# Optimization experiments

Hardware: AMD Instinct MI355X
Metric: run time of the kernel (lower is better)

## Reference

```python
import math
import jax, jax.numpy as jnp
import numpy as np

WS = (8, 7, 7)   # window_size (d, h, w)
SS = (4, 3, 3)   # shift_size
NH = 4           # num_heads
DIM = 128


def _rel_position_index(ws):
    # [N*N] int index into the (2wd-1)(2wh-1)(2ww-1) bias table
    cd, ch, cw = np.arange(ws[0]), np.arange(ws[1]), np.arange(ws[2])
    coords = np.stack(np.meshgrid(cd, ch, cw, indexing='ij')).reshape(3, -1)  # [3, N]
    rel = (coords[:, :, None] - coords[:, None, :]).transpose(1, 2, 0)        # [N, N, 3]
    rel[..., 0] += ws[0] - 1
    rel[..., 1] += ws[1] - 1
    rel[..., 2] += ws[2] - 1
    rel[..., 0] *= (2 * ws[1] - 1) * (2 * ws[2] - 1)
    rel[..., 1] *= (2 * ws[2] - 1)
    return rel.sum(-1).reshape(-1)


def _rel_coords_table(ws):
    # [(2wd-1)(2wh-1)(2ww-1), 3] log-spaced continuous coords (Swin v2)
    rd = np.arange(-(ws[0] - 1), ws[0], dtype=np.float32)
    rh = np.arange(-(ws[1] - 1), ws[1], dtype=np.float32)
    rw = np.arange(-(ws[2] - 1), ws[2], dtype=np.float32)
    t = np.stack(np.meshgrid(rd, rh, rw, indexing='ij')).transpose(1, 2, 3, 0)  # [Td,Th,Tw,3]
    t[..., 0] /= ws[0] - 1
    t[..., 1] /= ws[1] - 1
    t[..., 2] /= ws[2] - 1
    t *= 8.0
    t = np.sign(t) * np.log2(np.abs(t) + 1.0) / 3.0
    return t.reshape(-1, 3)


_REL_INDEX = _rel_position_index(WS)
_COORDS = jnp.asarray(_rel_coords_table(WS))


def _attn_mask(pD, pH, pW, ws, ss):
    img = np.zeros((pD, pH, pW), np.float32)
    sl = lambda w, s: (slice(0, -w), slice(-w, -s), slice(-s, None))
    cnt = 0
    for d in sl(ws[0], ss[0]):
        for h in sl(ws[1], ss[1]):
            for w in sl(ws[2], ss[2]):
                img[d, h, w] = cnt
                cnt += 1
    m = img.reshape(pD // ws[0], ws[0], pH // ws[1], ws[1], pW // ws[2], ws[2])
    m = m.transpose(0, 2, 4, 1, 3, 5).reshape(-1, ws[0] * ws[1] * ws[2])  # [nWin, N]
    diff = m[:, None, :] - m[:, :, None]
    return jnp.asarray(np.where(diff != 0, -100.0, 0.0).astype(np.float32))


def setup_inputs() -> dict:
    key = jax.random.key(0)
    ks = jax.random.split(key, 6)
    B, D, H, W, C = 1, 16, 56, 56, DIM
    g = lambda k, shp, sc: jax.random.normal(k, shp, dtype=jnp.float32) * sc
    return {
        'x': g(ks[0], (B, D, H, W, C), 1.0),
        'qkv_weight': g(ks[1], (3 * C, C), 0.02),
        'qkv_bias': jnp.zeros((3 * C,), jnp.float32),
        'proj_weight': g(ks[2], (C, C), 0.02),
        'proj_bias': jnp.zeros((C,), jnp.float32),
        'logit_scale': jnp.full((NH, 1, 1), float(np.log(10.0)), jnp.float32),
        'cpb_w1': g(ks[3], (512, 3), 0.02),
        'cpb_b1': jnp.zeros((512,), jnp.float32),
        'cpb_w2': g(ks[4], (NH, 512), 0.02),
    }


def reference(x, qkv_weight, qkv_bias, proj_weight, proj_bias,
              logit_scale, cpb_w1, cpb_b1, cpb_w2):
    B, D, H, W, C = x.shape
    wd, wh, ww = WS
    hd = C // NH
    pad_d, pad_h, pad_w = (-D) % wd, (-H) % wh, (-W) % ww
    x = jnp.pad(x, ((0, 0), (0, pad_d), (0, pad_h), (0, pad_w), (0, 0)))
    pD, pH, pW = D + pad_d, H + pad_h, W + pad_w
    ss = [0 if WS[i] >= (pD, pH, pW)[i] else SS[i] for i in range(3)]
    shifted = sum(ss) > 0
    if shifted:
        x = jnp.roll(x, (-ss[0], -ss[1], -ss[2]), axis=(1, 2, 3))
    nd, nh, nw = pD // wd, pH // wh, pW // ww
    nWin, N = nd * nh * nw, wd * wh * ww
    # window partition -> [B*nWin, N, C]
    xw = x.reshape(B, nd, wd, nh, wh, nw, ww, C).transpose(0, 1, 3, 5, 2, 4, 6, 7)
    xw = xw.reshape(B * nWin, N, C)
    # qkv with k-bias zeroed (Swin v2 cosine attention)
    qb = qkv_bias.at[C:2 * C].set(0.0)
    qkv = (xw @ qkv_weight.T + qb).reshape(B * nWin, N, 3, NH, hd).transpose(2, 0, 3, 1, 4)
    q, k, v = qkv[0], qkv[1], qkv[2]   # each [B*nWin, NH, N, hd]
    qn = q / jnp.maximum(jnp.linalg.norm(q, axis=-1, keepdims=True), 1e-12)
    kn = k / jnp.maximum(jnp.linalg.norm(k, axis=-1, keepdims=True), 1e-12)
    attn = jnp.einsum('bhnd,bhmd->bhnm', qn, kn)
    scale = jnp.exp(jnp.minimum(logit_scale, math.log(100.0)))  # [NH,1,1]
    attn = attn * scale
    # continuous relative position bias
    table = jax.nn.relu(_COORDS @ cpb_w1.T + cpb_b1) @ cpb_w2.T  # [T, NH]
    bias = table[_REL_INDEX].reshape(N, N, NH).transpose(2, 0, 1)
    bias = 16.0 * jax.nn.sigmoid(bias)
    attn = attn + bias[None]
    if shifted:
        mask = _attn_mask(pD, pH, pW, WS, ss)  # [nWin, N, N]
        attn = attn.reshape(B, nWin, NH, N, N) + mask[None, :, None]
        attn = attn.reshape(B * nWin, NH, N, N)
    attn = jax.nn.softmax(attn, axis=-1)
    out = jnp.einsum('bhnm,bhmd->bhnd', attn, v).transpose(0, 2, 1, 3).reshape(B * nWin, N, C)
    out = out @ proj_weight.T + proj_bias
    # window reverse -> [B, pD, pH, pW, C]
    out = out.reshape(B, nd, nh, nw, wd, wh, ww, C).transpose(0, 1, 4, 2, 5, 3, 6, 7)
    out = out.reshape(B, pD, pH, pW, C)
    if shifted:
        out = jnp.roll(out, tuple(ss), axis=(1, 2, 3))
    return out[:, :D, :H, :W, :]
```

## Files before the change

kernel.cpp:

```cpp
#include <hip/hip_runtime.h>
#include <hip/hip_bf16.h>

typedef unsigned short u16;
typedef unsigned int   u32;
typedef float f32x4  __attribute__((ext_vector_type(4)));
typedef short bf16x8 __attribute__((ext_vector_type(8)));

#define DI __device__ __forceinline__

constexpr int TBL  = 2535;
constexpr int NTOK = 50176;
constexpr float L2E = 1.4426950408889634f;

constexpr int WB_QW = 0;
constexpr int WB_PW = 49152;
constexpr int WB_QB = 65536;
constexpr int WB_PB = 65920;
constexpr int WB_TOT = 66048;

DI float b2f(u16 u){ return __uint_as_float(((u32)u)<<16); }
DI u16 f2b(float f){
  u32 u = __float_as_uint(f);
  return (u16)((u + 0x7fffu + ((u>>16)&1u)) >> 16);
}
DI float ldf(const void* p, int i, int isf32){
  return isf32 ? ((const float*)p)[i] : b2f(((const u16*)p)[i]);
}
DI f32x4 mfma16(bf16x8 a, bf16x8 b, f32x4 c){
  return __builtin_amdgcn_mfma_f32_16x16x32_bf16(a, b, c, 0, 0, 0);
}
DI u32 cvtpk(float lo, float hi){
  u32 r;
  asm("v_cvt_pk_bf16_f32 %0, %1, %2" : "=v"(r) : "v"(lo), "v"(hi));
  return r;
}
DI float vexp2(float x){
  float r;
  asm("v_exp_f32 %0, %1" : "=v"(r) : "v"(x));
  return r;
}
DI int detect_f32(const void* x, int lane){
  u32 w = ((const u32*)x)[lane];
  u16 lo = (u16)w;
  u32 e = (lo >> 7) & 0xFF;
  int wild = (lo != 0 && (e >= 143 || e <= 111)) ? 1 : 0;
  unsigned long long m = __ballot(wild);
  return __popcll(m) > 16;
}

__global__ void k_cpb(const void* __restrict__ w1, const void* __restrict__ b1,
                      const void* __restrict__ w2, const void* __restrict__ x,
                      const void* __restrict__ qw, const void* __restrict__ pw,
                      const void* __restrict__ qb, const void* __restrict__ pb,
                      u16* __restrict__ wb, float* __restrict__ table16){
  const int lane = threadIdx.x;
  const int isf32 = detect_f32(x, lane);
  {
    int gid = blockIdx.x*64 + lane;
    if (gid < WB_TOT){
      const void* src; int off;
      if (gid < WB_PW)      { src = qw; off = gid; }
      else if (gid < WB_QB) { src = pw; off = gid - WB_PW; }
      else if (gid < WB_PB) { src = qb; off = gid - WB_QB; }
      else                  { src = pb; off = gid - WB_PB; }
      wb[gid] = isf32 ? f2b(((const float*)src)[off]) : ((const u16*)src)[off];
    }
  }
  int t = blockIdx.x;
  int i = t/169; int r = t - i*169; int j = r/13; int k = r - j*13;
  float v0 = 8.f*(float)(i-7)/7.f, v1 = 8.f*(float)(j-6)/6.f, v2 = 8.f*(float)(k-6)/6.f;
  float c0 = copysignf(log2f(fabsf(v0)+1.f)*(1.f/3.f), v0);
  float c1 = copysignf(log2f(fabsf(v1)+1.f)*(1.f/3.f), v1);
  float c2 = copysignf(log2f(fabsf(v2)+1.f)*(1.f/3.f), v2);
  float a0=0.f,a1=0.f,a2=0.f,a3=0.f;
  for (int hh = lane; hh < 512; hh += 64){
    float a = c0*ldf(w1,hh*3,isf32) + c1*ldf(w1,hh*3+1,isf32)
            + c2*ldf(w1,hh*3+2,isf32) + ldf(b1,hh,isf32);
    a = fmaxf(a, 0.f);
    a0 += a*ldf(w2,hh,isf32);       a1 += a*ldf(w2,512+hh,isf32);
    a2 += a*ldf(w2,1024+hh,isf32);  a3 += a*ldf(w2,1536+hh,isf32);
  }
  #pragma unroll
  for (int off=32; off; off>>=1){
    a0 += __shfl_xor(a0, off); a1 += __shfl_xor(a1, off);
    a2 += __shfl_xor(a2, off); a3 += __shfl_xor(a3, off);
  }
  if (lane==0){
    table16[t]       = (16.f/(1.f+__expf(-a0)) - 15.f)*L2E;
    table16[TBL+t]   = (16.f/(1.f+__expf(-a1)) - 15.f)*L2E;
    table16[2*TBL+t] = (16.f/(1.f+__expf(-a2)) - 15.f)*L2E;
    table16[3*TBL+t] = (16.f/(1.f+__expf(-a3)) - 15.f)*L2E;
  }
}

__global__ void k_bias(const float* __restrict__ table16, float* __restrict__ bias16){
  int n = blockIdx.x, h = blockIdx.y;
  int td = n/49; int r2 = n - td*49; int th = r2/7; int tw = r2 - th*7;
  const float* tb = table16 + h*TBL;
  float* o = bias16 + ((size_t)h*392 + n)*392;
  for (int m = threadIdx.x; m < 392; m += 128){
    int sd = m/49; int q2 = m - sd*49; int sh = q2/7; int sw = q2 - sh*7;
    int idx = (td - sd + 7)*169 + (th - sh + 6)*13 + (tw - sw + 6);
    o[m] = tb[idx];
  }
}

__global__ __launch_bounds__(256,3) void k_qkv(const void* __restrict__ x,
    const u16* __restrict__ wb, const void* __restrict__ lsc,
    u16* __restrict__ qkvbuf){
  __shared__ __align__(16) u16 As[64*136];
  __shared__ __align__(16) u16 Ws[128*136];
  const int tid = threadIdx.x;
  const int lane = tid & 63;
  const int isf32 = detect_f32(x, lane);
  const int tokbase0 = blockIdx.x*64;
  {
    int trow = tid>>2, cq = (tid&3)*32;
    int gtok = tokbase0 + trow;
    int win = gtok/392, tt = gtok - win*392;
    int dwi = win>>6, hwi = (win>>3)&7, wwi = win&7;
    int td = tt/49; int r2 = tt - td*49; int th = r2/7; int tw = r2 - th*7;
    int pd = dwi*8 + td + 4; if (pd >= 16) pd -= 16;
    int ph = hwi*7 + th + 3; if (ph >= 56) ph -= 56;
    int pw = wwi*7 + tw + 3; if (pw >= 56) pw -= 56;
    size_t pos = (size_t)((pd*56 + ph)*56 + pw)*128 + cq;
    if (isf32){
      const float4* src = (const float4*)((const float*)x + pos);
      #pragma unroll
      for (int u=0; u<8; ++u){
        float4 a = src[u];
        ushort4 s4 = make_ushort4(f2b(a.x), f2b(a.y), f2b(a.z), f2b(a.w));
        *(ushort4*)&As[trow*136 + cq + u*4] = s4;
      }
    } else {
      const uint4* src = (const uint4*)((const u16*)x + pos);
      #pragma unroll
      for (int u=0; u<4; ++u) *(uint4*)&As[trow*136 + cq + u*8] = src[u];
    }
  }
  const int wave = tid>>6;
  const int c = lane & 15, g = lane >> 4;
  float sl2e[4];
  #pragma unroll
  for (int h2=0; h2<4; ++h2){
    float ls = ldf(lsc, h2, isf32);
    sl2e[h2] = __expf(fminf(ls, 4.60517019f)) * L2E;
  }
  bf16x8 ka[4];
  for (int which = 0; which < 3; ++which){
    __syncthreads();
    {
      int orow = tid>>1, c2 = (tid&1)*64;
      const uint4* src = (const uint4*)(wb + WB_QW + (size_t)(which*128 + orow)*128 + c2);
      #pragma unroll
      for (int u=0; u<8; ++u) *(uint4*)&Ws[orow*136 + c2 + u*8] = src[u];
    }
    __syncthreads();
    if (which == 0){
      #pragma unroll
      for (int kk=0; kk<4; ++kk)
        ka[kk] = *(const bf16x8*)&As[(wave*16 + c)*136 + kk*32 + g*8];
    }
    f32x4 acc[8];
    #pragma unroll
    for (int nt=0; nt<8; ++nt) acc[nt] = 0.f;
    #pragma unroll
    for (int nt=0; nt<8; ++nt){
      #pragma unroll
      for (int kk=0; kk<4; ++kk){
        bf16x8 wf = *(const bf16x8*)&Ws[(nt*16 + c)*136 + kk*32 + g*8];
        acc[nt] = mfma16(ka[kk], wf, acc[nt]);
      }
    }
    if (which != 1){
      #pragma unroll
      for (int nt=0; nt<8; ++nt){
        float bv = b2f(wb[WB_QB + which*128 + nt*16 + c]);
        #pragma unroll
        for (int r=0;r<4;++r) acc[nt][r] += bv;
      }
    }
    if (which < 2){
      #pragma unroll
      for (int h2=0; h2<4; ++h2){
        f32x4 ss;
        #pragma unroll
        for (int r=0;r<4;++r)
          ss[r] = acc[2*h2][r]*acc[2*h2][r] + acc[2*h2+1][r]*acc[2*h2+1][r];
        #pragma unroll
        for (int off=1; off<16; off<<=1){
          #pragma unroll
          for (int r=0;r<4;++r) ss[r] += __shfl_xor(ss[r], off);
        }
        #pragma unroll
        for (int r=0;r<4;++r){
          float rn = rsqrtf(fmaxf(ss[r], 1e-24f));
          if (which == 0) rn *= sl2e[h2];
          acc[2*h2][r]   *= rn;
          acc[2*h2+1][r] *= rn;
        }
      }
    }
    __syncthreads();
    #pragma unroll
    for (int nt=0; nt<8; ++nt){
      #pragma unroll
      for (int r=0;r<4;++r)
        As[(wave*16 + 4*g + r)*136 + nt*16 + c] = f2b(acc[nt][r]);
    }
    __syncthreads();
    {
      const int tokl = tid>>2, seg = tid&3;
      u16* dst = qkvbuf + ((size_t)(which*4+seg)*NTOK + tokbase0 + tokl)*32;
      const u16* srcl = &As[tokl*136 + seg*32];
      #pragma unroll
      for (int u=0; u<4; ++u)
        *(uint4*)(dst + u*8) = *(const uint4*)(srcl + u*8);
    }
  }
}

DI bf16x8 ldK(const u16* klds, int jt, int c, int g){
  return *(const bf16x8*)&klds[(jt*16 + c)*40 + g*8];
}
DI float4 ldB(const float* brow, int jt, int g){
  int mbc = jt*16 + 4*g; if (mbc > 388) mbc = 388;
  return *(const float4*)(brow + mbc);
}
DI int4 ldC(const int* cnt, int jt, int g){
  int mbc = jt*16 + 4*g; if (mbc > 388) mbc = 388;
  return *(const int4*)&cnt[mbc];
}

#define QKT_BODY(JJ, TAIL, KF, BA, BB, CM, JT) do { \
  f32x4 tz = {0.f,0.f,0.f,0.f}; \
  f32x4 ta = mfma16(KF, qfa, tz); \
  f32x4 tb = mfma16(KF, qfb, tz); \
  float pa0 = vexp2(ta[0] + BA.x), pa1 = vexp2(ta[1] + BA.y); \
  float pa2 = vexp2(ta[2] + BA.z), pa3 = vexp2(ta[3] + BA.w); \
  float pb0 = vexp2(tb[0] + BB.x), pb1 = vexp2(tb[1] + BB.y); \
  float pb2 = vexp2(tb[2] + BB.z), pb3 = vexp2(tb[3] + BB.w); \
  if (MIXED){ \
    if (CM.x != cnA) pa0 = 0.f;  if (CM.y != cnA) pa1 = 0.f; \
    if (CM.z != cnA) pa2 = 0.f;  if (CM.w != cnA) pa3 = 0.f; \
    if (CM.x != cnB) pb0 = 0.f;  if (CM.y != cnB) pb1 = 0.f; \
    if (CM.z != cnB) pb2 = 0.f;  if (CM.w != cnB) pb3 = 0.f; \
  } \
  if (TAIL){ \
    const int mb = (JT)*16 + 4*g; \
    if (mb > 388){ pa0=0.f; pa1=0.f; pa2=0.f; pa3=0.f; \
                   pb0=0.f; pb1=0.f; pb2=0.f; pb3=0.f; } \
  } \
  uint2 wva, wvb; \
  wva.x = cvtpk(pa0,pa1); wva.y = cvtpk(pa2,pa3); \
  wvb.x = cvtpk(pb0,pb1); wvb.y = cvtpk(pb2,pb3); \
  *(uint2*)&psA[c*20 + (JJ)*8 + 2*g] = wva; \
  *(uint2*)&psB[c*20 + (JJ)*8 + 2*g] = wvb; \
} while(0)

#define PV_PAIR(MC) do { \
  bf16x8 pfa = *(const bf16x8*)&psA[c*20 + 4*g]; \
  bf16x8 pfb = *(const bf16x8*)&psB[c*20 + 4*g]; \
  bf16x8 va = *(const bf16x8*)&vT[c*424 + (MC)*32 + g*8]; \
  bf16x8 vb = *(const bf16x8*)&vT[(16+c)*424 + (MC)*32 + g*8]; \
  o0a = mfma16(va, pfa, o0a); o1a = mfma16(vb, pfa, o1a); o2a = mfma16(ones, pfa, o2a); \
  o0b = mfma16(va, pfb, o0b); o1b = mfma16(vb, pfb, o1b); o2b = mfma16(ones, pfb, o2b); \
} while(0)

template<bool MIXED>
DI void attn_main(const u16* __restrict__ qg, const float* __restrict__ bias_h,
                  const u16* klds, const u16* vT, u32* psA, u32* psB, const int* cnt,
                  u16* __restrict__ aout, int win, int h, int wave, int lane){
  const int c = lane & 15, g = lane >> 4;
  const short ob = 0x3F80;
  const bf16x8 ones = {ob,ob,ob,ob,ob,ob,ob,ob};
  const int4 zc = {0,0,0,0};
  for (int pp = wave; pp < 13; pp += 8){
    const int rta = 2*pp;
    const int rtb = (pp < 12) ? (2*pp+1) : 24;
    const bool hasB = (pp < 12);
    const int nbA = rta*16, nbB = rtb*16;
    const int ncA = (nbA + c < 392) ? (nbA + c) : 391;
    const int ncB = (nbB + c < 392) ? (nbB + c) : 391;
    const bf16x8 qfa = *(const bf16x8*)(qg + (size_t)ncA*32 + g*8);
    const bf16x8 qfb = *(const bf16x8*)(qg + (size_t)ncB*32 + g*8);
    const int cnA = MIXED ? cnt[ncA] : 0;
    const int cnB = MIXED ? cnt[ncB] : 0;
    const float* browA = bias_h + (size_t)ncA*392;
    const float* browB = bias_h + (size_t)ncB*392;
    f32x4 o0a = {0.f,0.f,0.f,0.f}, o1a = o0a, o2a = o0a;
    f32x4 o0b = o0a, o1b = o0a, o2b = o0a;
    bf16x8 kf0 = ldK(klds, 0, c, g);
    float4 ba0 = ldB(browA, 0, g), bb0 = ldB(browB, 0, g);
    int4   cm0 = MIXED ? ldC(cnt, 0, g) : zc;
    for (int mc = 0; mc < 12; ++mc){
      const int jt1 = 2*mc + 1, jt2 = 2*mc + 2;
      bf16x8 kf1 = ldK(klds, jt1, c, g);
      float4 ba1 = ldB(browA, jt1, g), bb1 = ldB(browB, jt1, g);
      int4   cm1 = MIXED ? ldC(cnt, jt1, g) : zc;
      QKT_BODY(0, false, kf0, ba0, bb0, cm0, 2*mc);
      kf0 = ldK(klds, jt2, c, g);
      ba0 = ldB(browA, jt2, g); bb0 = ldB(browB, jt2, g);
      cm0 = MIXED ? ldC(cnt, jt2, g) : zc;
      QKT_BODY(1, false, kf1, ba1, bb1, cm1, jt1);
      PV_PAIR(mc);
    }
    QKT_BODY(0, true, kf0, ba0, bb0, cm0, 24);
    { uint2 zz; zz.x = 0u; zz.y = 0u;
      *(uint2*)&psA[c*20 + 8 + 2*g] = zz;
      *(uint2*)&psB[c*20 + 8 + 2*g] = zz; }
    PV_PAIR(12);
    const float rva = 1.f / o2a[0];
    const float rvb = 1.f / o2b[0];
    uint2 wa, wb2;
    wa.x  = cvtpk(o0a[0]*rva, o0a[1]*rva);  wa.y  = cvtpk(o0a[2]*rva, o0a[3]*rva);
    wb2.x = cvtpk(o1a[0]*rva, o1a[1]*rva);  wb2.y = cvtpk(o1a[2]*rva, o1a[3]*rva);
    *(uint2*)&psA[c*20 + 2*g]     = wa;
    *(uint2*)&psA[c*20 + 8 + 2*g] = wb2;
    wa.x  = cvtpk(o0b[0]*rvb, o0b[1]*rvb);  wa.y  = cvtpk(o0b[2]*rvb, o0b[3]*rvb);
    wb2.x = cvtpk(o1b[0]*rvb, o1b[1]*rvb);  wb2.y = cvtpk(o1b[2]*rvb, o1b[3]*rvb);
    *(uint2*)&psB[c*20 + 2*g]     = wa;
    *(uint2*)&psB[c*20 + 8 + 2*g] = wb2;
    const int orow = lane>>2, oq = lane&3;
    uint4 ova = *(const uint4*)&psA[orow*20 + 4*oq];
    const int nA = nbA + orow;
    if (nA < 392)
      *(uint4*)(aout + ((size_t)(win*392 + nA))*128 + h*32 + oq*8) = ova;
    if (hasB){
      uint4 ovb = *(const uint4*)&psB[orow*20 + 4*oq];
      const int nB = nbB + orow;
      if (nB < 392)
        *(uint4*)(aout + ((size_t)(win*392 + nB))*128 + h*32 + oq*8) = ovb;
    }
  }
}

__global__ __launch_bounds__(512,4) void k_attn(const u16* __restrict__ qkv,
    const float* __restrict__ bias16, u16* __restrict__ aout){
  __shared__ __align__(16) u16 klds[400*40];
  __shared__ __align__(16) u16 vT[32*424];
  __shared__ __align__(16) u32 ps[8][640];
  __shared__ __align__(16) int cnt[400];
  const int tid = threadIdx.x;
  const int win = blockIdx.x, h = blockIdx.y;
  const int dwi = win>>6, hwi = (win>>3)&7, wwi = win&7;
  const u16* qg = qkv + ((size_t)(0*4 + h)*NTOK + (size_t)win*392)*32;
  const u16* kg = qkv + ((size_t)(1*4 + h)*NTOK + (size_t)win*392)*32;
  const u16* vg = qkv + ((size_t)(2*4 + h)*NTOK + (size_t)win*392)*32;
  for (int idx = tid; idx < 1600; idx += 512){
    const int row = idx>>2, q = idx&3;
    uint4 a = {0,0,0,0};
    if (row < 392) a = *(const uint4*)(kg + (size_t)row*32 + q*8);
    *(uint4*)&klds[row*40 + q*8] = a;
  }
  for (int idx = tid; idx < 784; idx += 512){
    const int mg = idx>>3, cg = idx&7;
    uint2 v0 = *(const uint2*)(vg + (size_t)(4*mg+0)*32 + cg*4);
    uint2 v1 = *(const uint2*)(vg + (size_t)(4*mg+1)*32 + cg*4);
    uint2 v2 = *(const uint2*)(vg + (size_t)(4*mg+2)*32 + cg*4);
    uint2 v3 = *(const uint2*)(vg + (size_t)(4*mg+3)*32 + cg*4);
    u16 e0[4], e1[4], e2[4], e3[4];
    e0[0]=(u16)v0.x; e0[1]=(u16)(v0.x>>16); e0[2]=(u16)v0.y; e0[3]=(u16)(v0.y>>16);
    e1[0]=(u16)v1.x; e1[1]=(u16)(v1.x>>16); e1[2]=(u16)v1.y; e1[3]=(u16)(v1.y>>16);
    e2[0]=(u16)v2.x; e2[1]=(u16)(v2.x>>16); e2[2]=(u16)v2.y; e2[3]=(u16)(v2.y>>16);
    e3[0]=(u16)v3.x; e3[1]=(u16)(v3.x>>16); e3[2]=(u16)v3.y; e3[3]=(u16)(v3.y>>16);
    #pragma unroll
    for (int cc=0; cc<4; ++cc){
      ushort4 w = make_ushort4(e0[cc], e1[cc], e2[cc], e3[cc]);
      *(ushort4*)&vT[(cg*4+cc)*424 + 4*mg] = w;
    }
  }
  for (int idx = tid; idx < 1024; idx += 512){
    int ch = idx>>5, mm = 392 + (idx&31);
    vT[ch*424 + mm] = 0;
  }
  for (int t2 = tid; t2 < 400; t2 += 512){
    int row = (t2 < 392) ? t2 : 391;
    int td = row/49; int r2 = row - td*49; int th = r2/7; int tw = r2 - th*7;
    int gd = dwi*8 + td, gh = hwi*7 + th, gw = wwi*7 + tw;
    int rd = (gd < 8) ? 0 : ((gd < 12) ? 1 : 2);
    int rh = (gh < 49) ? 0 : ((gh < 53) ? 1 : 2);
    int rw = (gw < 49) ? 0 : ((gw < 53) ? 1 : 2);
    cnt[t2] = rd*9 + rh*3 + rw;
  }
  __syncthreads();
  const int wave = tid>>6, lane = tid&63;
  u32* psA = &ps[wave][0];
  u32* psB = &ps[wave][320];
  const float* bias_h = bias16 + (size_t)h*153664;
  const bool uniform = (dwi == 0) && (hwi < 7) && (wwi < 7);
  if (uniform)
    attn_main<false>(qg, bias_h, klds, vT, psA, psB, cnt, aout, win, h, wave, lane);
  else
    attn_main<true >(qg, bias_h, klds, vT, psA, psB, cnt, aout, win, h, wave, lane);
}

__global__ __launch_bounds__(256,2) void k_proj(const u16* __restrict__ ain,
    const u16* __restrict__ wb, const void* __restrict__ x, void* __restrict__ out){
  __shared__ __align__(16) u16 As[64*136];
  __shared__ __align__(16) u16 Ws[128*136];
  const int tid = threadIdx.x;
  const int lane = tid & 63;
  const int isf32 = detect_f32(x, lane);
  const int tokbase0 = blockIdx.x*64;
  {
    int trow = tid>>2, cq = (tid&3)*32;
    const uint4* src = (const uint4*)(ain + (size_t)(tokbase0+trow)*128 + cq);
    #pragma unroll
    for (int u=0; u<4; ++u) *(uint4*)&As[trow*136 + cq + u*8] = src[u];
  }
  {
    int orow = tid>>1, c2 = (tid&1)*64;
    const uint4* src = (const uint4*)(wb + WB_PW + (size_t)orow*128 + c2);
    #pragma unroll
    for (int u=0; u<8; ++u) *(uint4*)&Ws[orow*136 + c2 + u*8] = src[u];
  }
  __syncthreads();
  const int wave = tid>>6;
  const int c = lane & 15, g = lane >> 4;
  bf16x8 ka[4];
  #pragma unroll
  for (int kk=0; kk<4; ++kk)
    ka[kk] = *(const bf16x8*)&As[(wave*16 + c)*136 + kk*32 + g*8];
  f32x4 acc[8];
  #pragma unroll
  for (int nt=0; nt<8; ++nt) acc[nt] = 0.f;
  #pragma unroll
  for (int nt=0; nt<8; ++nt){
    #pragma unroll
    for (int kk=0; kk<4; ++kk){
      bf16x8 wf = *(const bf16x8*)&Ws[(nt*16 + c)*136 + kk*32 + g*8];
      acc[nt] = mfma16(ka[kk], wf, acc[nt]);
    }
  }
  if (isf32){
    __syncthreads();
    float* WsF = (float*)Ws;
    #pragma unroll
    for (int nt=0; nt<8; ++nt){
      float bv = b2f(wb[WB_PB + nt*16 + c]);
      #pragma unroll
      for (int r=0;r<4;++r)
        WsF[(wave*16 + 4*g + r)*128 + nt*16 + c] = acc[nt][r] + bv;
    }
    __syncthreads();
    const int tok = tid>>2, q4 = tid&3;
    int gtok = tokbase0 + tok;
    int win = gtok/392, tt = gtok - win*392;
    int dwi = win>>6, hwi = (win>>3)&7, wwi = win&7;
    int td = tt/49; int r2 = tt - td*49; int th = r2/7; int tw = r2 - th*7;
    int pd = dwi*8 + td + 4; if (pd >= 16) pd -= 16;
    int ph = hwi*7 + th + 3; if (ph >= 56) ph -= 56;
    int pwx = wwi*7 + tw + 3; if (pwx >= 56) pwx -= 56;
    size_t po = (size_t)((pd*56 + ph)*56 + pwx)*128;
    const float4* srcv = (const float4*)&WsF[tok*128 + q4*32];
    float4* dst = (float4*)((float*)out + po + q4*32);
    #pragma unroll
    for (int i=0;i<8;++i) dst[i] = srcv[i];
  } else {
    const int tokbase = tokbase0 + wave*16;
    size_t po[4];
    #pragma unroll
    for (int r=0;r<4;++r){
      int gtok = tokbase + 4*g + r;
      int win = gtok/392, tt = gtok - win*392;
      int dwi = win>>6, hwi = (win>>3)&7, wwi = win&7;
      int td = tt/49; int r2 = tt - td*49; int th = r2/7; int tw = r2 - th*7;
      int pd = dwi*8 + td + 4; if (pd >= 16) pd -= 16;
      int ph = hwi*7 + th + 3; if (ph >= 56) ph -= 56;
      int pwx = wwi*7 + tw + 3; if (pwx >= 56) pwx -= 56;
      po[r] = (size_t)((pd*56 + ph)*56 + pwx)*128;
    }
    #pragma unroll
    for (int nt=0; nt<8; ++nt){
      int oc = nt*16 + c;
      float bv = b2f(wb[WB_PB + oc]);
      #pragma unroll
      for (int r=0;r<4;++r)
        ((u16*)out)[po[r] + oc] = f2b(acc[nt][r] + bv);
    }
  }
}

extern "C" void kernel_launch(void* const* d_in, const int* in_sizes, int n_in,
                              void* d_out, int out_size, void* d_ws, size_t ws_size,
                              hipStream_t stream){
  const void* x      = d_in[0];
  const void* qkv_w  = d_in[1];
  const void* qkv_b  = d_in[2];
  const void* proj_w = d_in[3];
  const void* proj_b = d_in[4];
  const void* lsc    = d_in[5];
  const void* cpb_w1 = d_in[6];
  const void* cpb_b1 = d_in[7];
  const void* cpb_w2 = d_in[8];
  char* ws = (char*)d_ws;
  float* table16 = (float*)(ws);
  float* bias16  = (float*)(ws + 40960);
  u16*   wb      = (u16*)(ws + 2499584);
  u16*   qkvbuf  = (u16*)(ws + 2631680);
  u16*   attnout = (u16*)(ws + 41166848);

  k_cpb <<<TBL, 64, 0, stream>>>(cpb_w1, cpb_b1, cpb_w2, x,
                                 qkv_w, proj_w, qkv_b, proj_b, wb, table16);
  k_bias<<<dim3(392,4), 128, 0, stream>>>(table16, bias16);
  k_qkv <<<784, 256, 0, stream>>>(x, wb, lsc, qkvbuf);
  k_attn<<<dim3(128,4), 512, 0, stream>>>(qkvbuf, bias16, attnout);
  k_proj<<<784, 256, 0, stream>>>(attnout, wb, x, d_out);
}
```

Before: 105.5 us.

## Load QKV input fragments directly from global and drop As LDS staging

The QKV projection kernel now has each wave load its 16 token rows straight from global memory into MFMA A fragments, converting fp32 to bf16 with packed converts. This removes the As shared-memory tile and its barriers. The output is now written with scalar 2-byte global stores per element instead of being staged through LDS for coalesced 16-byte writes, and launch bounds are raised to 4 blocks per CU to use the freed LDS. The risk is uncoalesced input loads and many narrow scattered output stores. The mfma16 helper is also renamed to mfma32.

Result: faster. 94.89 us (-10.0%).

```diff
diff --git a/kernel.cpp b/kernel.cpp
--- a/kernel.cpp
+++ b/kernel.cpp
@@ -26,7 +26,7 @@
 DI float ldf(const void* p, int i, int isf32){
   return isf32 ? ((const float*)p)[i] : b2f(((const u16*)p)[i]);
 }
-DI f32x4 mfma16(bf16x8 a, bf16x8 b, f32x4 c){
+DI f32x4 mfma32(bf16x8 a, bf16x8 b, f32x4 c){
   return __builtin_amdgcn_mfma_f32_16x16x32_bf16(a, b, c, 0, 0, 0);
 }
 DI u32 cvtpk(float lo, float hi){
@@ -105,50 +105,52 @@
   }
 }
 
-__global__ __launch_bounds__(256,3) void k_qkv(const void* __restrict__ x,
+__global__ __launch_bounds__(256,4) void k_qkv(const void* __restrict__ x,
     const u16* __restrict__ wb, const void* __restrict__ lsc,
     u16* __restrict__ qkvbuf){
-  __shared__ __align__(16) u16 As[64*136];
   __shared__ __align__(16) u16 Ws[128*136];
   const int tid = threadIdx.x;
   const int lane = tid & 63;
   const int isf32 = detect_f32(x, lane);
-  const int tokbase0 = blockIdx.x*64;
+  const int wave = tid>>6;
+  const int c = lane & 15, g = lane >> 4;
+  const int tokbase = blockIdx.x*64 + wave*16;
+  bf16x8 ka[4];
   {
-    int trow = tid>>2, cq = (tid&3)*32;
-    int gtok = tokbase0 + trow;
+    int gtok = tokbase + c;
     int win = gtok/392, tt = gtok - win*392;
     int dwi = win>>6, hwi = (win>>3)&7, wwi = win&7;
     int td = tt/49; int r2 = tt - td*49; int th = r2/7; int tw = r2 - th*7;
     int pd = dwi*8 + td + 4; if (pd >= 16) pd -= 16;
     int ph = hwi*7 + th + 3; if (ph >= 56) ph -= 56;
     int pw = wwi*7 + tw + 3; if (pw >= 56) pw -= 56;
-    size_t pos = (size_t)((pd*56 + ph)*56 + pw)*128 + cq;
+    size_t rowb = (size_t)((pd*56 + ph)*56 + pw)*128;
     if (isf32){
-      const float4* src = (const float4*)((const float*)x + pos);
-      #pragma unroll
-      for (int u=0; u<8; ++u){
-        float4 a = src[u];
-        ushort4 s4 = make_ushort4(f2b(a.x), f2b(a.y), f2b(a.z), f2b(a.w));
-        *(ushort4*)&As[trow*136 + cq + u*4] = s4;
+      const float* xr = (const float*)x + rowb + g*8;
+      #pragma unroll
+      for (int kk=0; kk<4; ++kk){
+        float4 f0 = *(const float4*)(xr + kk*32);
+        float4 f1 = *(const float4*)(xr + kk*32 + 4);
+        uint4 p;
+        p.x = cvtpk(f0.x, f0.y);  p.y = cvtpk(f0.z, f0.w);
+        p.z = cvtpk(f1.x, f1.y);  p.w = cvtpk(f1.z, f1.w);
+        ka[kk] = *(bf16x8*)&p;
       }
     } else {
-      const uint4* src = (const uint4*)((const u16*)x + pos);
-      #pragma unroll
-      for (int u=0; u<4; ++u) *(uint4*)&As[trow*136 + cq + u*8] = src[u];
-    }
-  }
-  const int wave = tid>>6;
-  const int c = lane & 15, g = lane >> 4;
+      const u16* xr = (const u16*)x + rowb + g*8;
+      #pragma unroll
+      for (int kk=0; kk<4; ++kk)
+        ka[kk] = *(const bf16x8*)(xr + kk*32);
+    }
+  }
   float sl2e[4];
   #pragma unroll
   for (int h2=0; h2<4; ++h2){
     float ls = ldf(lsc, h2, isf32);
     sl2e[h2] = __expf(fminf(ls, 4.60517019f)) * L2E;
   }
-  bf16x8 ka[4];
   for (int which = 0; which < 3; ++which){
-    __syncthreads();
+    if (which) __syncthreads();
     {
       int orow = tid>>1, c2 = (tid&1)*64;
       const uint4* src = (const uint4*)(wb + WB_QW + (size_t)(which*128 + orow)*128 + c2);
@@ -156,11 +158,6 @@
       for (int u=0; u<8; ++u) *(uint4*)&Ws[orow*136 + c2 + u*8] = src[u];
     }
     __syncthreads();
-    if (which == 0){
-      #pragma unroll
-      for (int kk=0; kk<4; ++kk)
-        ka[kk] = *(const bf16x8*)&As[(wave*16 + c)*136 + kk*32 + g*8];
-    }
     f32x4 acc[8];
     #pragma unroll
     for (int nt=0; nt<8; ++nt) acc[nt] = 0.f;
@@ -169,7 +166,7 @@
       #pragma unroll
       for (int kk=0; kk<4; ++kk){
         bf16x8 wf = *(const bf16x8*)&Ws[(nt*16 + c)*136 + kk*32 + g*8];
-        acc[nt] = mfma16(ka[kk], wf, acc[nt]);
+        acc[nt] = mfma32(ka[kk], wf, acc[nt]);
       }
     }
     if (which != 1){
@@ -201,21 +198,15 @@
         }
       }
     }
-    __syncthreads();
     #pragma unroll
     for (int nt=0; nt<8; ++nt){
-      #pragma unroll
-      for (int r=0;r<4;++r)
-        As[(wave*16 + 4*g + r)*136 + nt*16 + c] = f2b(acc[nt][r]);
-    }
-    __syncthreads();
-    {
-      const int tokl = tid>>2, seg = tid&3;
-      u16* dst = qkvbuf + ((size_t)(which*4+seg)*NTOK + tokbase0 + tokl)*32;
-      const u16* srcl = &As[tokl*136 + seg*32];
-      #pragma unroll
-      for (int u=0; u<4; ++u)
-        *(uint4*)(dst + u*8) = *(const uint4*)(srcl + u*8);
+      int oc = nt*16 + c;
+      int head = oc >> 5, chb = oc & 31;
+      #pragma unroll
+      for (int r=0;r<4;++r){
+        int t = tokbase + 4*g + r;
+        qkvbuf[((size_t)(which*4+head)*NTOK + t)*32 + chb] = f2b(acc[nt][r]);
+      }
     }
   }
 }
@@ -234,8 +225,8 @@
 
 #define QKT_BODY(JJ, TAIL, KF, BA, BB, CM, JT) do { \
   f32x4 tz = {0.f,0.f,0.f,0.f}; \
-  f32x4 ta = mfma16(KF, qfa, tz); \
-  f32x4 tb = mfma16(KF, qfb, tz); \
+  f32x4 ta = mfma32(KF, qfa, tz); \
+  f32x4 tb = mfma32(KF, qfb, tz); \
   float pa0 = vexp2(ta[0] + BA.x), pa1 = vexp2(ta[1] + BA.y); \
   float pa2 = vexp2(ta[2] + BA.z), pa3 = vexp2(ta[3] + BA.w); \
   float pb0 = vexp2(tb[0] + BB.x), pb1 = vexp2(tb[1] + BB.y); \
@@ -263,8 +254,8 @@
   bf16x8 pfb = *(const bf16x8*)&psB[c*20 + 4*g]; \
   bf16x8 va = *(const bf16x8*)&vT[c*424 + (MC)*32 + g*8]; \
   bf16x8 vb = *(const bf16x8*)&vT[(16+c)*424 + (MC)*32 + g*8]; \
-  o0a = mfma16(va, pfa, o0a); o1a = mfma16(vb, pfa, o1a); o2a = mfma16(ones, pfa, o2a); \
-  o0b = mfma16(va, pfb, o0b); o1b = mfma16(vb, pfb, o1b); o2b = mfma16(ones, pfb, o2b); \
+  o0a = mfma32(va, pfa, o0a); o1a = mfma32(vb, pfa, o1a); o2a = mfma32(ones, pfa, o2a); \
+  o0b = mfma32(va, pfb, o0b); o1b = mfma32(vb, pfb, o1b); o2b = mfma32(ones, pfb, o2b); \
 } while(0)
 
 template<bool MIXED>
@@ -430,7 +421,7 @@
     #pragma unroll
     for (int kk=0; kk<4; ++kk){
       bf16x8 wf = *(const bf16x8*)&Ws[(nt*16 + c)*136 + kk*32 + g*8];
-      acc[nt] = mfma16(ka[kk], wf, acc[nt]);
+      acc[nt] = mfma32(ka[kk], wf, acc[nt]);
     }
   }
   if (isf32){
```
